# Optimization experiments

Measured on AMD Instinct MI355X. Metric: run time of the kernel, lower is better.

Reference implementation:

```python
import jax, jax.numpy as jnp
import numpy as np

N = 20000
E = 320000
IN_DIM, HID, MID, OUT, HEADS = 1536, 512, 128, 5, 8
NEG_SLOPE = 0.2
BN_EPS = 1e-5


def gat_conv(x, edge_index, W, a_src, a_dst, bias, heads, out_ch):
    """PyG-style GATConv (eval mode, self-loops already in edge_index).
    x: [N, F_in]; W: [F_in, heads*out_ch]; a_src/a_dst: [heads, out_ch]; bias: [heads*out_ch].
    Returns [N, heads*out_ch] (head concat)."""
    n = x.shape[0]
    h = (x @ W).reshape(n, heads, out_ch)              # [N,H,C]
    src, dst = edge_index[0], edge_index[1]
    al_s = jnp.sum(h * a_src, axis=-1)                 # [N,H]
    al_d = jnp.sum(h * a_dst, axis=-1)                 # [N,H]
    e = al_s[src] + al_d[dst]                          # [E,H]
    e = jnp.where(e >= 0, e, NEG_SLOPE * e)            # leaky_relu
    # segment softmax over incoming edges per dst node
    e_max = jax.ops.segment_max(e, dst, num_segments=n)
    e_max = jnp.where(jnp.isfinite(e_max), e_max, 0.0)
    ex = jnp.exp(e - e_max[dst])                       # [E,H]
    denom = jax.ops.segment_sum(ex, dst, num_segments=n)
    alpha = ex / (denom[dst] + 1e-16)                  # [E,H]
    msg = h[src] * alpha[:, :, None]                   # [E,H,C]
    out = jax.ops.segment_sum(msg, dst, num_segments=n)
    return out.reshape(n, heads * out_ch) + bias


def bn_eval(x, gamma, beta, mean, var):
    return (x - mean) * jax.lax.rsqrt(var + BN_EPS) * gamma + beta


def setup_inputs() -> dict:
    key = jax.random.key(0)
    ks = jax.random.split(key, 24)
    x = jax.random.normal(ks[0], (N, IN_DIM), dtype=jnp.float32)
    edge_index = jax.random.randint(ks[1], (2, E), 0, N, dtype=jnp.int32)

    def glorot(k, shape):
        fan = shape[0] + shape[-1]
        return jax.random.normal(k, shape, dtype=jnp.float32) * np.sqrt(2.0 / fan)

    inp = {"x": x, "edge_index": edge_index}
    # conv1: 1536 -> 8 heads x 64
    inp["W1"] = glorot(ks[2], (IN_DIM, HID))
    inp["as1"] = glorot(ks[3], (HEADS, HID // HEADS))
    inp["ad1"] = glorot(ks[4], (HEADS, HID // HEADS))
    inp["b1"] = jnp.zeros((HID,), jnp.float32)
    # conv2: 512 -> 8 heads x 16
    inp["W2"] = glorot(ks[5], (HID, MID))
    inp["as2"] = glorot(ks[6], (HEADS, MID // HEADS))
    inp["ad2"] = glorot(ks[7], (HEADS, MID // HEADS))
    inp["b2"] = jnp.zeros((MID,), jnp.float32)
    # conv3: 128 -> 1 head x 5
    inp["W3"] = glorot(ks[8], (MID, OUT))
    inp["as3"] = glorot(ks[9], (1, OUT))
    inp["ad3"] = glorot(ks[10], (1, OUT))
    inp["b3"] = jnp.zeros((OUT,), jnp.float32)
    # batchnorm params (eval mode, running stats)
    inp["g1"] = jax.random.normal(ks[11], (HID,), jnp.float32) * 0.1 + 1.0
    inp["be1"] = jax.random.normal(ks[12], (HID,), jnp.float32) * 0.1
    inp["m1"] = jax.random.normal(ks[13], (HID,), jnp.float32) * 0.1
    inp["v1"] = jax.random.uniform(ks[14], (HID,), jnp.float32, 0.5, 1.5)
    inp["g2"] = jax.random.normal(ks[15], (MID,), jnp.float32) * 0.1 + 1.0
    inp["be2"] = jax.random.normal(ks[16], (MID,), jnp.float32) * 0.1
    inp["m2"] = jax.random.normal(ks[17], (MID,), jnp.float32) * 0.1
    inp["v2"] = jax.random.uniform(ks[18], (MID,), jnp.float32, 0.5, 1.5)
    return inp


def reference(x, edge_index, W1, as1, ad1, b1, W2, as2, ad2, b2, W3, as3, ad3, b3,
              g1, be1, m1, v1, g2, be2, m2, v2):
    # add self-loops (PyG GATConv default)
    loops = jnp.arange(N, dtype=edge_index.dtype)
    ei = jnp.concatenate([edge_index, jnp.stack([loops, loops])], axis=1)

    h = jax.nn.relu(gat_conv(x, ei, W1, as1, ad1, b1, HEADS, HID // HEADS))
    h = bn_eval(h, g1, be1, m1, v1)
    h = jax.nn.relu(gat_conv(h, ei, W2, as2, ad2, b2, HEADS, MID // HEADS))
    h = bn_eval(h, g2, be2, m2, v2)
    h = gat_conv(h, ei, W3, as3, ad3, b3, 1, OUT)
    return jax.nn.log_softmax(h, axis=1)
```

## Files before the change

kernel.cpp:

```cpp
#include <hip/hip_runtime.h>
#include <math.h>

#define IN_DIM 1536
#define HID 512
#define MID 128
#define OUTC 5
#define HEADS 8
#define NEG_SLOPE 0.2f
#define BN_EPS 1e-5f

typedef __attribute__((ext_vector_type(8))) short s16x8;
typedef __attribute__((ext_vector_type(4))) float fx4;

__device__ __forceinline__ unsigned short bf16_rne(float f) {
    unsigned int u = __float_as_uint(f);
    u += 0x7fffu + ((u >> 16) & 1u);
    return (unsigned short)(u >> 16);
}
__device__ __forceinline__ float bf16_to_f32(unsigned short u) {
    return __uint_as_float((unsigned int)u << 16);
}

__device__ __forceinline__ void async_copy16(void* lds, const void* g) {
    __builtin_amdgcn_global_load_lds(
        (const __attribute__((address_space(1))) unsigned int*)g,
        (__attribute__((address_space(3))) unsigned int*)lds, 16, 0, 0);
}

__global__ void hist_kernel(const int* __restrict__ ei, int* __restrict__ deg,
                            int ET, int E) {
    int e = blockIdx.x * blockDim.x + threadIdx.x;
    if (e >= ET) return;
    int dst = (e < E) ? ei[E + e] : (e - E);
    atomicAdd(&deg[dst], 1);
}

__global__ __launch_bounds__(1024) void scan_kernel(const int* __restrict__ deg,
                                                    int* __restrict__ row_ptr,
                                                    int* __restrict__ cursor, int n) {
    __shared__ int partial[1024];
    int tid = threadIdx.x;
    int per = (n + 1023) / 1024;
    int base = tid * per;
    int s = 0;
    for (int i = 0; i < per; ++i) {
        int idx = base + i;
        if (idx < n) s += deg[idx];
    }
    partial[tid] = s;
    __syncthreads();
    for (int off = 1; off < 1024; off <<= 1) {
        int v = (tid >= off) ? partial[tid - off] : 0;
        __syncthreads();
        partial[tid] += v;
        __syncthreads();
    }
    int prefix = (tid == 0) ? 0 : partial[tid - 1];
    for (int i = 0; i < per; ++i) {
        int idx = base + i;
        if (idx < n) {
            row_ptr[idx] = prefix;
            cursor[idx] = prefix;
            prefix += deg[idx];
        }
    }
    if (tid == 1023) row_ptr[n] = partial[1023];
}

__global__ void scatter_kernel(const int* __restrict__ ei, int* __restrict__ cursor,
                               int* __restrict__ csr_src, int ET, int E) {
    int e = blockIdx.x * blockDim.x + threadIdx.x;
    if (e >= ET) return;
    int src, dst;
    if (e < E) { src = ei[e]; dst = ei[E + e]; }
    else       { src = dst = e - E; }
    int slot = atomicAdd(&cursor[dst], 1);
    csr_src[slot] = src;
}

__global__ void cvt_bf16_kernel(const float* __restrict__ in,
                                unsigned short* __restrict__ out, int n4) {
    int i = blockIdx.x * blockDim.x + threadIdx.x;
    if (i >= n4) return;
    float4 v = ((const float4*)in)[i];
    ushort4 o;
    o.x = bf16_rne(v.x); o.y = bf16_rne(v.y);
    o.z = bf16_rne(v.z); o.w = bf16_rne(v.w);
    ((ushort4*)out)[i] = o;
}

template <bool WLO>
__global__ __launch_bounds__(256) void transpose_split(
    const float* __restrict__ W, unsigned short* __restrict__ Th,
    unsigned short* __restrict__ Tl, int K, int Nn) {
    __shared__ float tile[32][33];
    int kb = blockIdx.y * 32, nb = blockIdx.x * 32;
    int tx = threadIdx.x & 31, ty = threadIdx.x >> 5;
#pragma unroll
    for (int r = 0; r < 4; ++r)
        tile[ty + r * 8][tx] = W[(size_t)(kb + ty + r * 8) * Nn + nb + tx];
    __syncthreads();
#pragma unroll
    for (int r = 0; r < 4; ++r) {
        int n = ty + r * 8;
        float v = tile[tx][n];
        unsigned short hi = bf16_rne(v);
        size_t o = (size_t)(nb + n) * K + kb + tx;
        Th[o] = hi;
        if (WLO) {
            float hif = __uint_as_float((unsigned int)hi << 16);
            Tl[o] = bf16_rne(v - hif);
        }
    }
}

__global__ __launch_bounds__(256) void gemm1_kernel(
    const unsigned short* __restrict__ A, const unsigned short* __restrict__ Bh,
    unsigned short* __restrict__ Cb, int M, int N, int K, int MBLK) {
    int b = blockIdx.x;
    int xm = (b & 7) + 8 * (b >> 5);
    int ym = (b >> 3) & 3;
    if (xm >= MBLK) return;

    __shared__ unsigned short Asb[2][128 * 32];
    __shared__ unsigned short Bsb[2][128 * 32];

    const int tid = threadIdx.x;
    const int lane = tid & 63;
    const int wv = tid >> 6;
    const int row0 = xm * 128;
    const int nb0 = ym * 128;
    const int col = lane & 15;
    const int quad = lane >> 4;
    const int m0 = (wv >> 1) * 64;
    const int n0 = (wv & 1) * 64;

    const int s_row = lane >> 2;
    const int s_chunk = (lane & 3) ^ ((lane >> 3) & 3);
    int agr0 = row0 + (wv * 2 + 0) * 16 + s_row; if (agr0 >= M) agr0 = M - 1;
    int agr1 = row0 + (wv * 2 + 1) * 16 + s_row; if (agr1 >= M) agr1 = M - 1;
    const size_t ag0 = (size_t)agr0 * K + s_chunk * 8;
    const size_t ag1 = (size_t)agr1 * K + s_chunk * 8;
    const size_t bg0 = (size_t)(nb0 + (wv * 2 + 0) * 16 + s_row) * K + s_chunk * 8;
    const size_t bg1 = (size_t)(nb0 + (wv * 2 + 1) * 16 + s_row) * K + s_chunk * 8;

    const int rsw = (col >> 1) & 3;

    fx4 acc[4][4];
#pragma unroll
    for (int i = 0; i < 4; ++i)
#pragma unroll
        for (int j = 0; j < 4; ++j) acc[i][j] = (fx4){0.f, 0.f, 0.f, 0.f};

    async_copy16(&Asb[0][(wv * 2 + 0) * 512], A + ag0);
    async_copy16(&Asb[0][(wv * 2 + 1) * 512], A + ag1);
    async_copy16(&Bsb[0][(wv * 2 + 0) * 512], Bh + bg0);
    async_copy16(&Bsb[0][(wv * 2 + 1) * 512], Bh + bg1);
    __syncthreads();

    int cur = 0;
    for (int k0 = 0; k0 < K; k0 += 32) {
        const int nxt = cur ^ 1;
        if (k0 + 32 < K) {
            const int kn = k0 + 32;
            async_copy16(&Asb[nxt][(wv * 2 + 0) * 512], A + ag0 + kn);
            async_copy16(&Asb[nxt][(wv * 2 + 1) * 512], A + ag1 + kn);
            async_copy16(&Bsb[nxt][(wv * 2 + 0) * 512], Bh + bg0 + kn);
            async_copy16(&Bsb[nxt][(wv * 2 + 1) * 512], Bh + bg1 + kn);
        }
        s16x8 afr[4], bfr[4];
#pragma unroll
        for (int i = 0; i < 4; ++i)
            afr[i] = *(const s16x8*)&Asb[cur][(m0 + i * 16 + col) * 32 + (quad ^ rsw) * 8];
#pragma unroll
        for (int j = 0; j < 4; ++j)
            bfr[j] = *(const s16x8*)&Bsb[cur][(n0 + j * 16 + col) * 32 + (quad ^ rsw) * 8];
#pragma unroll
        for (int i = 0; i < 4; ++i)
#pragma unroll
            for (int j = 0; j < 4; ++j)
                acc[i][j] = __builtin_amdgcn_mfma_f32_16x16x32_bf16(afr[i], bfr[j], acc[i][j], 0, 0, 0);
        __syncthreads();
        cur = nxt;
    }

#pragma unroll
    for (int i = 0; i < 4; ++i) {
        int gr0 = row0 + m0 + i * 16 + quad * 4;
#pragma unroll
        for (int j = 0; j < 4; ++j) {
            int gc = nb0 + n0 + j * 16 + col;
#pragma unroll
            for (int r = 0; r < 4; ++r) {
                int gr = gr0 + r;
                if (gr < M) Cb[(size_t)gr * N + gc] = bf16_rne(acc[i][j][r]);
            }
        }
    }
}

__global__ __launch_bounds__(256) void gemm2_kernel(
    const unsigned short* __restrict__ A, const unsigned short* __restrict__ Bh,
    const unsigned short* __restrict__ Bl, unsigned short* __restrict__ Cb,
    int M, int N, int K) {
    __shared__ unsigned short Asb[2][32 * 32];
    __shared__ unsigned short Bhb[2][128 * 32];
    __shared__ unsigned short Blb[2][128 * 32];

    const int tid = threadIdx.x;
    const int lane = tid & 63;
    const int wv = tid >> 6;
    const int row0 = blockIdx.x * 32;
    const int col = lane & 15;
    const int quad = lane >> 4;
    const int m0 = (wv >> 1) * 16;
    const int n0 = (wv & 1) * 64;
    const int b_row = lane >> 2;
    const int b_chunk = (lane & 3) ^ ((lane >> 3) & 3);
    const int rsw = (col >> 1) & 3;

    const int t0 = wv * 2, t1 = t0 + 1;
    const size_t bgo0 = (size_t)(t0 * 16 + b_row) * K + b_chunk * 8;
    const size_t bgo1 = (size_t)(t1 * 16 + b_row) * K + b_chunk * 8;
    int agr = row0 + wv * 16 + b_row; if (agr >= M) agr = M - 1;
    const size_t ago = (size_t)agr * K + b_chunk * 8;

    fx4 acc[4];
#pragma unroll
    for (int j = 0; j < 4; ++j) acc[j] = (fx4){0.f, 0.f, 0.f, 0.f};

    auto stage = [&](int buf, int k) {
        async_copy16(&Bhb[buf][t0 * 512], Bh + bgo0 + k);
        async_copy16(&Bhb[buf][t1 * 512], Bh + bgo1 + k);
        async_copy16(&Blb[buf][t0 * 512], Bl + bgo0 + k);
        async_copy16(&Blb[buf][t1 * 512], Bl + bgo1 + k);
        if (wv < 2) async_copy16(&Asb[buf][wv * 512], A + ago + k);
    };

    stage(0, 0);
    __syncthreads();

    int cur = 0;
    for (int k0 = 0; k0 < K; k0 += 32) {
        const int nxt = cur ^ 1;
        if (k0 + 32 < K) stage(nxt, k0 + 32);
        s16x8 a, bh4[4], bl4[4];
        a = *(const s16x8*)&Asb[cur][(m0 + col) * 32 + (quad ^ rsw) * 8];
#pragma unroll
        for (int j = 0; j < 4; ++j) {
            int rb = (n0 + j * 16 + col) * 32 + (quad ^ rsw) * 8;
            bh4[j] = *(const s16x8*)&Bhb[cur][rb];
            bl4[j] = *(const s16x8*)&Blb[cur][rb];
        }
#pragma unroll
        for (int j = 0; j < 4; ++j) {
            acc[j] = __builtin_amdgcn_mfma_f32_16x16x32_bf16(a, bl4[j], acc[j], 0, 0, 0);
            acc[j] = __builtin_amdgcn_mfma_f32_16x16x32_bf16(a, bh4[j], acc[j], 0, 0, 0);
        }
        __syncthreads();
        cur = nxt;
    }

    int gr0 = row0 + m0 + quad * 4;
#pragma unroll
    for (int j = 0; j < 4; ++j) {
        int gc = n0 + j * 16 + col;
#pragma unroll
        for (int r = 0; r < 4; ++r) {
            int gr = gr0 + r;
            if (gr < M) Cb[(size_t)gr * N + gc] = bf16_rne(acc[j][r]);
        }
    }
}

template <int H, int C>
__global__ void alsd_kernel(const unsigned short* __restrict__ hlin,
                            const float* __restrict__ a_s,
                            const float* __restrict__ a_d, float* __restrict__ als,
                            float* __restrict__ ald, int n) {
    int t = blockIdx.x * blockDim.x + threadIdx.x;
    if (t >= n * H) return;
    int node = t / H, h = t % H;
    const unsigned short* row = hlin + (size_t)node * H * C + h * C;
    const float* asr = a_s + h * C;
    const float* adr = a_d + h * C;
    float ss = 0.f, sd = 0.f;
#pragma unroll
    for (int c0 = 0; c0 < C; c0 += 4) {
        ushort4 u = *(const ushort4*)&row[c0];
        float v0 = bf16_to_f32(u.x), v1 = bf16_to_f32(u.y);
        float v2 = bf16_to_f32(u.z), v3 = bf16_to_f32(u.w);
        ss += v0 * asr[c0] + v1 * asr[c0 + 1] + v2 * asr[c0 + 2] + v3 * asr[c0 + 3];
        sd += v0 * adr[c0] + v1 * adr[c0 + 1] + v2 * adr[c0 + 2] + v3 * adr[c0 + 3];
    }
    als[t] = ss;
    ald[t] = sd;
}

template <int F, int VEC, bool SPLIT>
__global__ __launch_bounds__(128) void agg_fused_kernel(
    const unsigned short* __restrict__ hlin, const float* __restrict__ als,
    const float* __restrict__ ald, const int* __restrict__ row_ptr,
    const int* __restrict__ csr_src, const float* __restrict__ bias,
    const float* __restrict__ gamma, const float* __restrict__ beta,
    const float* __restrict__ mean, const float* __restrict__ var,
    float* __restrict__ outf, unsigned short* __restrict__ outh) {
    int dst = blockIdx.x;
    int tid = threadIdx.x;
    int f0 = tid * VEC;
    int h = tid >> 4;
    __shared__ float exs[16][8];
    __shared__ int srcs[16];
    int s0 = row_ptr[dst], s1 = row_ptr[dst + 1];
    int cj = tid >> 3, ch = tid & 7;
    float ald_c = ald[dst * HEADS + ch];
    float acc[VEC];
#pragma unroll
    for (int v = 0; v < VEC; ++v) acc[v] = 0.f;
    float den = 0.f;

    for (int base = s0; base < s1; base += 16) {
        int take = min(16, s1 - base);
        if (cj < take) {
            int src = csr_src[base + cj];
            if (ch == 0) srcs[cj] = src;
            float e = als[src * HEADS + ch] + ald_c;
            e = (e >= 0.f) ? e : NEG_SLOPE * e;
            exs[cj][ch] = __expf(e);
        }
        __syncthreads();
        for (int jj = 0; jj < take; ++jj) {
            int src = srcs[jj];
            float a = exs[jj][h];
            den += a;
            const unsigned short* rp = &hlin[(size_t)src * F + f0];
            if (VEC == 4) {
                ushort4 u = *(const ushort4*)rp;
                acc[0] += a * bf16_to_f32(u.x);
                acc[1] += a * bf16_to_f32(u.y);
                acc[2] += a * bf16_to_f32(u.z);
                acc[3] += a * bf16_to_f32(u.w);
            } else {
                acc[0] += a * bf16_to_f32(rp[0]);
            }
        }
        __syncthreads();
    }

    float rd = 1.f / (den + 1e-16f);
    float res[VEC];
#pragma unroll
    for (int v = 0; v < VEC; ++v) {
        int f = f0 + v;
        float val = acc[v] * rd + bias[f];
        val = fmaxf(val, 0.f);
        val = (val - mean[f]) * rsqrtf(var[f] + BN_EPS) * gamma[f] + beta[f];
        res[v] = val;
    }
    if (SPLIT) {
        if (VEC == 4) {
            ushort4 o;
            o.x = bf16_rne(res[0]); o.y = bf16_rne(res[1]);
            o.z = bf16_rne(res[2]); o.w = bf16_rne(res[3]);
            *(ushort4*)&outh[(size_t)dst * F + f0] = o;
        } else {
            outh[(size_t)dst * F + f0] = bf16_rne(res[0]);
        }
    } else {
        if (VEC == 4) {
            *(float4*)&outf[(size_t)dst * F + f0] =
                make_float4(res[0], res[1], res[2], res[3]);
        } else {
            outf[(size_t)dst * F + f0] = res[0];
        }
    }
}

__global__ void layer3_lin_kernel(const float* __restrict__ h2, const float* __restrict__ W3,
                                  const float* __restrict__ as3, const float* __restrict__ ad3,
                                  float* __restrict__ h3lin, float* __restrict__ als,
                                  float* __restrict__ ald, int n) {
    int node = blockIdx.x * blockDim.x + threadIdx.x;
    if (node >= n) return;
    const float* row = h2 + (size_t)node * MID;
    float acc[OUTC] = {0.f, 0.f, 0.f, 0.f, 0.f};
    for (int k = 0; k < MID; ++k) {
        float x = row[k];
#pragma unroll
        for (int c = 0; c < OUTC; ++c) acc[c] += x * W3[k * OUTC + c];
    }
    float ss = 0.f, sd = 0.f;
#pragma unroll
    for (int c = 0; c < OUTC; ++c) {
        h3lin[(size_t)node * OUTC + c] = acc[c];
        ss += acc[c] * as3[c];
        sd += acc[c] * ad3[c];
    }
    als[node] = ss;
    ald[node] = sd;
}

__global__ void agg3_lsm_kernel(const float* __restrict__ h3lin, const float* __restrict__ als,
                                const float* __restrict__ ald, const int* __restrict__ row_ptr,
                                const int* __restrict__ csr_src, const float* __restrict__ b3,
                                float* __restrict__ out, int n) {
    int dst = blockIdx.x * blockDim.x + threadIdx.x;
    if (dst >= n) return;
    int s0 = row_ptr[dst], s1 = row_ptr[dst + 1];
    float ad = ald[dst];
    float den = 0.f;
    float acc[OUTC] = {0.f, 0.f, 0.f, 0.f, 0.f};
    for (int j = s0; j < s1; ++j) {
        int src = csr_src[j];
        float e = als[src] + ad;
        e = (e >= 0.f) ? e : NEG_SLOPE * e;
        float x = __expf(e);
        den += x;
#pragma unroll
        for (int c = 0; c < OUTC; ++c) acc[c] += x * h3lin[(size_t)src * OUTC + c];
    }
    float rd = 1.f / (den + 1e-16f);
    float m = -INFINITY;
#pragma unroll
    for (int c = 0; c < OUTC; ++c) {
        acc[c] = acc[c] * rd + b3[c];
        m = fmaxf(m, acc[c]);
    }
    float s = 0.f;
#pragma unroll
    for (int c = 0; c < OUTC; ++c) s += __expf(acc[c] - m);
    float lse = m + __logf(s);
#pragma unroll
    for (int c = 0; c < OUTC; ++c) out[(size_t)dst * OUTC + c] = acc[c] - lse;
}

extern "C" void kernel_launch(void* const* d_in, const int* in_sizes, int n_in,
                              void* d_out, int out_size, void* d_ws, size_t ws_size,
                              hipStream_t stream) {
    const float* x   = (const float*)d_in[0];
    const int*   ei  = (const int*)d_in[1];
    const float* W1  = (const float*)d_in[2];
    const float* as1 = (const float*)d_in[3];
    const float* ad1 = (const float*)d_in[4];
    const float* b1  = (const float*)d_in[5];
    const float* W2  = (const float*)d_in[6];
    const float* as2 = (const float*)d_in[7];
    const float* ad2 = (const float*)d_in[8];
    const float* b2  = (const float*)d_in[9];
    const float* W3  = (const float*)d_in[10];
    const float* as3 = (const float*)d_in[11];
    const float* ad3 = (const float*)d_in[12];
    const float* b3  = (const float*)d_in[13];
    const float* g1  = (const float*)d_in[14];
    const float* be1 = (const float*)d_in[15];
    const float* m1  = (const float*)d_in[16];
    const float* v1  = (const float*)d_in[17];
    const float* g2  = (const float*)d_in[18];
    const float* be2 = (const float*)d_in[19];
    const float* m2  = (const float*)d_in[20];
    const float* v2  = (const float*)d_in[21];

    const int N = in_sizes[0] / IN_DIM;
    const int E = in_sizes[1] / 2;
    const int ET = E + N;
    const int MBLK1 = (N + 127) / 128;
    const int MBLK2 = (N + 31) / 32;

    char* ws = (char*)d_ws;
    size_t off = 0;
    auto take = [&](size_t bytes) -> char* {
        char* p = ws + off;
        off += (bytes + 255) & ~(size_t)255;
        return p;
    };
    int* deg      = (int*)take((size_t)N * 4);
    int* row_ptr  = (int*)take((size_t)(N + 1) * 4);
    int* cursor   = (int*)take((size_t)N * 4);
    int* csr_src  = (int*)take((size_t)ET * 4);
    unsigned short* W1h = (unsigned short*)take((size_t)HID * IN_DIM * 2);
    unsigned short* W2h = (unsigned short*)take((size_t)MID * HID * 2);
    unsigned short* W2l = (unsigned short*)take((size_t)MID * HID * 2);
    unsigned short* xh  = (unsigned short*)take((size_t)N * IN_DIM * 2);
    unsigned short* h1lin = (unsigned short*)take((size_t)N * HID * 2);
    unsigned short* h1h   = (unsigned short*)take((size_t)N * HID * 2);
    unsigned short* h2lin = (unsigned short*)take((size_t)N * MID * 2);
    float* h2post = (float*)take((size_t)N * MID * 4);
    float* h3lin  = (float*)take((size_t)N * OUTC * 4);
    float* als    = (float*)take((size_t)N * HEADS * 4);
    float* ald    = (float*)take((size_t)N * HEADS * 4);

    hipMemsetAsync(deg, 0, (size_t)N * 4, stream);
    hist_kernel<<<(ET + 255) / 256, 256, 0, stream>>>(ei, deg, ET, E);
    scan_kernel<<<1, 1024, 0, stream>>>(deg, row_ptr, cursor, N);
    scatter_kernel<<<(ET + 255) / 256, 256, 0, stream>>>(ei, cursor, csr_src, ET, E);
    transpose_split<false><<<dim3(HID / 32, IN_DIM / 32), 256, 0, stream>>>(
        W1, W1h, nullptr, IN_DIM, HID);
    transpose_split<true><<<dim3(MID / 32, HID / 32), 256, 0, stream>>>(
        W2, W2h, W2l, HID, MID);
    {
        int n4 = N * IN_DIM / 4;
        cvt_bf16_kernel<<<(n4 + 255) / 256, 256, 0, stream>>>(x, xh, n4);
    }

    gemm1_kernel<<<640, 256, 0, stream>>>(xh, W1h, h1lin, N, HID, IN_DIM, MBLK1);
    alsd_kernel<HEADS, 64><<<(N * HEADS + 255) / 256, 256, 0, stream>>>(h1lin, as1, ad1, als, ald, N);
    agg_fused_kernel<HID, 4, true><<<N, 128, 0, stream>>>(
        h1lin, als, ald, row_ptr, csr_src, b1, g1, be1, m1, v1, nullptr, h1h);

    gemm2_kernel<<<MBLK2, 256, 0, stream>>>(h1h, W2h, W2l, h2lin, N, MID, HID);
    alsd_kernel<HEADS, 16><<<(N * HEADS + 255) / 256, 256, 0, stream>>>(h2lin, as2, ad2, als, ald, N);
    agg_fused_kernel<MID, 1, false><<<N, 128, 0, stream>>>(
        h2lin, als, ald, row_ptr, csr_src, b2, g2, be2, m2, v2, h2post, nullptr);

    layer3_lin_kernel<<<(N + 255) / 256, 256, 0, stream>>>(
        h2post, W3, as3, ad3, h3lin, als, ald, N);
    agg3_lsm_kernel<<<(N + 255) / 256, 256, 0, stream>>>(
        h3lin, als, ald, row_ptr, csr_src, b3, (float*)d_out, N);
}
```

Measured before the change: 467.4 us.

## Fuse attention logits into GEMM epilogues and layer-3 linear into layer-2 aggregation

```diff
diff --git a/kernel.cpp b/kernel.cpp
--- a/kernel.cpp
+++ b/kernel.cpp
@@ -116,7 +116,9 @@
 
 __global__ __launch_bounds__(256) void gemm1_kernel(
     const unsigned short* __restrict__ A, const unsigned short* __restrict__ Bh,
-    unsigned short* __restrict__ Cb, int M, int N, int K, int MBLK) {
+    unsigned short* __restrict__ Cb, const float* __restrict__ a_s,
+    const float* __restrict__ a_d, float* __restrict__ als,
+    float* __restrict__ ald, int M, int N, int K, int MBLK) {
     int b = blockIdx.x;
     int xm = (b & 7) + 8 * (b >> 5);
     int ym = (b >> 3) & 3;
@@ -197,12 +199,43 @@
             }
         }
     }
+
+    const int head = (nb0 + n0) >> 6;
+    float asv[4], adv[4];
+#pragma unroll
+    for (int j = 0; j < 4; ++j) {
+        asv[j] = a_s[head * 64 + j * 16 + col];
+        adv[j] = a_d[head * 64 + j * 16 + col];
+    }
+#pragma unroll
+    for (int i = 0; i < 4; ++i) {
+#pragma unroll
+        for (int r = 0; r < 4; ++r) {
+            float ss = acc[i][0][r] * asv[0] + acc[i][1][r] * asv[1] +
+                       acc[i][2][r] * asv[2] + acc[i][3][r] * asv[3];
+            float sd = acc[i][0][r] * adv[0] + acc[i][1][r] * adv[1] +
+                       acc[i][2][r] * adv[2] + acc[i][3][r] * adv[3];
+#pragma unroll
+            for (int off = 8; off; off >>= 1) {
+                ss += __shfl_xor(ss, off);
+                sd += __shfl_xor(sd, off);
+            }
+            if (col == 0) {
+                int gr = row0 + m0 + i * 16 + quad * 4 + r;
+                if (gr < M) {
+                    als[gr * HEADS + head] = ss;
+                    ald[gr * HEADS + head] = sd;
+                }
+            }
+        }
+    }
 }
 
 __global__ __launch_bounds__(256) void gemm2_kernel(
     const unsigned short* __restrict__ A, const unsigned short* __restrict__ Bh,
     const unsigned short* __restrict__ Bl, unsigned short* __restrict__ Cb,
-    int M, int N, int K) {
+    const float* __restrict__ a_s, const float* __restrict__ a_d,
+    float* __restrict__ als, float* __restrict__ ald, int M, int N, int K) {
     __shared__ unsigned short Asb[2][32 * 32];
     __shared__ unsigned short Bhb[2][128 * 32];
     __shared__ unsigned short Blb[2][128 * 32];
@@ -271,40 +304,44 @@
             if (gr < M) Cb[(size_t)gr * N + gc] = bf16_rne(acc[j][r]);
         }
     }
-}
-
-template <int H, int C>
-__global__ void alsd_kernel(const unsigned short* __restrict__ hlin,
-                            const float* __restrict__ a_s,
-                            const float* __restrict__ a_d, float* __restrict__ als,
-                            float* __restrict__ ald, int n) {
-    int t = blockIdx.x * blockDim.x + threadIdx.x;
-    if (t >= n * H) return;
-    int node = t / H, h = t % H;
-    const unsigned short* row = hlin + (size_t)node * H * C + h * C;
-    const float* asr = a_s + h * C;
-    const float* adr = a_d + h * C;
-    float ss = 0.f, sd = 0.f;
-#pragma unroll
-    for (int c0 = 0; c0 < C; c0 += 4) {
-        ushort4 u = *(const ushort4*)&row[c0];
-        float v0 = bf16_to_f32(u.x), v1 = bf16_to_f32(u.y);
-        float v2 = bf16_to_f32(u.z), v3 = bf16_to_f32(u.w);
-        ss += v0 * asr[c0] + v1 * asr[c0 + 1] + v2 * asr[c0 + 2] + v3 * asr[c0 + 3];
-        sd += v0 * adr[c0] + v1 * adr[c0 + 1] + v2 * adr[c0 + 2] + v3 * adr[c0 + 3];
-    }
-    als[t] = ss;
-    ald[t] = sd;
-}
-
-template <int F, int VEC, bool SPLIT>
+
+    float asv[4], adv[4];
+#pragma unroll
+    for (int j = 0; j < 4; ++j) {
+        asv[j] = a_s[n0 + j * 16 + col];
+        adv[j] = a_d[n0 + j * 16 + col];
+    }
+#pragma unroll
+    for (int j = 0; j < 4; ++j) {
+        int head = (n0 >> 4) + j;
+#pragma unroll
+        for (int r = 0; r < 4; ++r) {
+            float ss = acc[j][r] * asv[j];
+            float sd = acc[j][r] * adv[j];
+#pragma unroll
+            for (int off = 8; off; off >>= 1) {
+                ss += __shfl_xor(ss, off);
+                sd += __shfl_xor(sd, off);
+            }
+            if (col == 0) {
+                int gr = gr0 + r;
+                if (gr < M) {
+                    als[gr * HEADS + head] = ss;
+                    ald[gr * HEADS + head] = sd;
+                }
+            }
+        }
+    }
+}
+
+template <int F, int VEC>
 __global__ __launch_bounds__(128) void agg_fused_kernel(
     const unsigned short* __restrict__ hlin, const float* __restrict__ als,
     const float* __restrict__ ald, const int* __restrict__ row_ptr,
     const int* __restrict__ csr_src, const float* __restrict__ bias,
     const float* __restrict__ gamma, const float* __restrict__ beta,
     const float* __restrict__ mean, const float* __restrict__ var,
-    float* __restrict__ outf, unsigned short* __restrict__ outh) {
+    unsigned short* __restrict__ outh) {
     int dst = blockIdx.x;
     int tid = threadIdx.x;
     int f0 = tid * VEC;
@@ -334,104 +371,144 @@
             float a = exs[jj][h];
             den += a;
             const unsigned short* rp = &hlin[(size_t)src * F + f0];
-            if (VEC == 4) {
-                ushort4 u = *(const ushort4*)rp;
-                acc[0] += a * bf16_to_f32(u.x);
-                acc[1] += a * bf16_to_f32(u.y);
-                acc[2] += a * bf16_to_f32(u.z);
-                acc[3] += a * bf16_to_f32(u.w);
-            } else {
-                acc[0] += a * bf16_to_f32(rp[0]);
-            }
+            ushort4 u = *(const ushort4*)rp;
+            acc[0] += a * bf16_to_f32(u.x);
+            acc[1] += a * bf16_to_f32(u.y);
+            acc[2] += a * bf16_to_f32(u.z);
+            acc[3] += a * bf16_to_f32(u.w);
         }
         __syncthreads();
     }
 
     float rd = 1.f / (den + 1e-16f);
-    float res[VEC];
+    ushort4 o;
+    unsigned short* op = (unsigned short*)&o;
 #pragma unroll
     for (int v = 0; v < VEC; ++v) {
         int f = f0 + v;
         float val = acc[v] * rd + bias[f];
         val = fmaxf(val, 0.f);
         val = (val - mean[f]) * rsqrtf(var[f] + BN_EPS) * gamma[f] + beta[f];
-        res[v] = val;
-    }
-    if (SPLIT) {
-        if (VEC == 4) {
-            ushort4 o;
-            o.x = bf16_rne(res[0]); o.y = bf16_rne(res[1]);
-            o.z = bf16_rne(res[2]); o.w = bf16_rne(res[3]);
-            *(ushort4*)&outh[(size_t)dst * F + f0] = o;
-        } else {
-            outh[(size_t)dst * F + f0] = bf16_rne(res[0]);
-        }
-    } else {
-        if (VEC == 4) {
-            *(float4*)&outf[(size_t)dst * F + f0] =
-                make_float4(res[0], res[1], res[2], res[3]);
-        } else {
-            outf[(size_t)dst * F + f0] = res[0];
-        }
-    }
-}
-
-__global__ void layer3_lin_kernel(const float* __restrict__ h2, const float* __restrict__ W3,
-                                  const float* __restrict__ as3, const float* __restrict__ ad3,
-                                  float* __restrict__ h3lin, float* __restrict__ als,
-                                  float* __restrict__ ald, int n) {
-    int node = blockIdx.x * blockDim.x + threadIdx.x;
-    if (node >= n) return;
-    const float* row = h2 + (size_t)node * MID;
-    float acc[OUTC] = {0.f, 0.f, 0.f, 0.f, 0.f};
-    for (int k = 0; k < MID; ++k) {
-        float x = row[k];
-#pragma unroll
-        for (int c = 0; c < OUTC; ++c) acc[c] += x * W3[k * OUTC + c];
-    }
-    float ss = 0.f, sd = 0.f;
-#pragma unroll
-    for (int c = 0; c < OUTC; ++c) {
-        h3lin[(size_t)node * OUTC + c] = acc[c];
-        ss += acc[c] * as3[c];
-        sd += acc[c] * ad3[c];
-    }
-    als[node] = ss;
-    ald[node] = sd;
-}
-
-__global__ void agg3_lsm_kernel(const float* __restrict__ h3lin, const float* __restrict__ als,
-                                const float* __restrict__ ald, const int* __restrict__ row_ptr,
-                                const int* __restrict__ csr_src, const float* __restrict__ b3,
-                                float* __restrict__ out, int n) {
-    int dst = blockIdx.x * blockDim.x + threadIdx.x;
+        op[v] = bf16_rne(val);
+    }
+    *(ushort4*)&outh[(size_t)dst * F + f0] = o;
+}
+
+__global__ __launch_bounds__(128) void agg2_l3_kernel(
+    const unsigned short* __restrict__ hlin, const float* __restrict__ als,
+    const float* __restrict__ ald, const int* __restrict__ row_ptr,
+    const int* __restrict__ csr_src, const float* __restrict__ bias,
+    const float* __restrict__ gamma, const float* __restrict__ beta,
+    const float* __restrict__ mean, const float* __restrict__ var,
+    const float* __restrict__ W3, const float* __restrict__ as3,
+    const float* __restrict__ ad3, float* __restrict__ h3lin,
+    float* __restrict__ als3, float* __restrict__ ald3) {
+    int dst = blockIdx.x;
+    int tid = threadIdx.x;
+    int h = tid >> 4;
+    __shared__ float exs[16][8];
+    __shared__ int srcs[16];
+    __shared__ float red[2][OUTC];
+    int s0 = row_ptr[dst], s1 = row_ptr[dst + 1];
+    int cj = tid >> 3, ch = tid & 7;
+    float ald_c = ald[dst * HEADS + ch];
+    float acc = 0.f, den = 0.f;
+
+    for (int base = s0; base < s1; base += 16) {
+        int take = min(16, s1 - base);
+        if (cj < take) {
+            int src = csr_src[base + cj];
+            if (ch == 0) srcs[cj] = src;
+            float e = als[src * HEADS + ch] + ald_c;
+            e = (e >= 0.f) ? e : NEG_SLOPE * e;
+            exs[cj][ch] = __expf(e);
+        }
+        __syncthreads();
+        for (int jj = 0; jj < take; ++jj) {
+            int src = srcs[jj];
+            float a = exs[jj][h];
+            den += a;
+            acc += a * bf16_to_f32(hlin[(size_t)src * MID + tid]);
+        }
+        __syncthreads();
+    }
+
+    float val = acc / (den + 1e-16f) + bias[tid];
+    val = fmaxf(val, 0.f);
+    val = (val - mean[tid]) * rsqrtf(var[tid] + BN_EPS) * gamma[tid] + beta[tid];
+
+    float p[OUTC];
+#pragma unroll
+    for (int c = 0; c < OUTC; ++c) p[c] = val * W3[tid * OUTC + c];
+#pragma unroll
+    for (int off = 32; off; off >>= 1) {
+#pragma unroll
+        for (int c = 0; c < OUTC; ++c) p[c] += __shfl_xor(p[c], off);
+    }
+    int wv = tid >> 6;
+    if ((tid & 63) == 0) {
+#pragma unroll
+        for (int c = 0; c < OUTC; ++c) red[wv][c] = p[c];
+    }
+    __syncthreads();
+    if (tid == 0) {
+        float ss = 0.f, sd = 0.f;
+#pragma unroll
+        for (int c = 0; c < OUTC; ++c) {
+            float v = red[0][c] + red[1][c];
+            h3lin[(size_t)dst * OUTC + c] = v;
+            ss += v * as3[c];
+            sd += v * ad3[c];
+        }
+        als3[dst] = ss;
+        ald3[dst] = sd;
+    }
+}
+
+__global__ __launch_bounds__(256) void agg3_lsm_kernel(
+    const float* __restrict__ h3lin, const float* __restrict__ als,
+    const float* __restrict__ ald, const int* __restrict__ row_ptr,
+    const int* __restrict__ csr_src, const float* __restrict__ b3,
+    float* __restrict__ out, int n) {
+    int g = blockIdx.x * blockDim.x + threadIdx.x;
+    int dst = g >> 4;
+    int l = g & 15;
     if (dst >= n) return;
     int s0 = row_ptr[dst], s1 = row_ptr[dst + 1];
     float ad = ald[dst];
     float den = 0.f;
     float acc[OUTC] = {0.f, 0.f, 0.f, 0.f, 0.f};
-    for (int j = s0; j < s1; ++j) {
+    for (int j = s0 + l; j < s1; j += 16) {
         int src = csr_src[j];
         float e = als[src] + ad;
         e = (e >= 0.f) ? e : NEG_SLOPE * e;
         float x = __expf(e);
         den += x;
-#pragma unroll
-        for (int c = 0; c < OUTC; ++c) acc[c] += x * h3lin[(size_t)src * OUTC + c];
-    }
-    float rd = 1.f / (den + 1e-16f);
-    float m = -INFINITY;
-#pragma unroll
-    for (int c = 0; c < OUTC; ++c) {
-        acc[c] = acc[c] * rd + b3[c];
-        m = fmaxf(m, acc[c]);
-    }
-    float s = 0.f;
-#pragma unroll
-    for (int c = 0; c < OUTC; ++c) s += __expf(acc[c] - m);
-    float lse = m + __logf(s);
-#pragma unroll
-    for (int c = 0; c < OUTC; ++c) out[(size_t)dst * OUTC + c] = acc[c] - lse;
+        const float* hp = h3lin + (size_t)src * OUTC;
+#pragma unroll
+        for (int c = 0; c < OUTC; ++c) acc[c] += x * hp[c];
+    }
+#pragma unroll
+    for (int off = 8; off; off >>= 1) {
+        den += __shfl_xor(den, off);
+#pragma unroll
+        for (int c = 0; c < OUTC; ++c) acc[c] += __shfl_xor(acc[c], off);
+    }
+    if (l == 0) {
+        float rd = 1.f / (den + 1e-16f);
+        float m = -INFINITY;
+#pragma unroll
+        for (int c = 0; c < OUTC; ++c) {
+            acc[c] = acc[c] * rd + b3[c];
+            m = fmaxf(m, acc[c]);
+        }
+        float s = 0.f;
+#pragma unroll
+        for (int c = 0; c < OUTC; ++c) s += __expf(acc[c] - m);
+        float lse = m + __logf(s);
+#pragma unroll
+        for (int c = 0; c < OUTC; ++c) out[(size_t)dst * OUTC + c] = acc[c] - lse;
+    }
 }
 
 extern "C" void kernel_launch(void* const* d_in, const int* in_sizes, int n_in,
@@ -484,10 +561,11 @@
     unsigned short* h1lin = (unsigned short*)take((size_t)N * HID * 2);
     unsigned short* h1h   = (unsigned short*)take((size_t)N * HID * 2);
     unsigned short* h2lin = (unsigned short*)take((size_t)N * MID * 2);
-    float* h2post = (float*)take((size_t)N * MID * 4);
     float* h3lin  = (float*)take((size_t)N * OUTC * 4);
     float* als    = (float*)take((size_t)N * HEADS * 4);
     float* ald    = (float*)take((size_t)N * HEADS * 4);
+    float* als3   = (float*)take((size_t)N * 4);
+    float* ald3   = (float*)take((size_t)N * 4);
 
     hipMemsetAsync(deg, 0, (size_t)N * 4, stream);
     hist_kernel<<<(ET + 255) / 256, 256, 0, stream>>>(ei, deg, ET, E);
@@ -502,18 +580,17 @@
         cvt_bf16_kernel<<<(n4 + 255) / 256, 256, 0, stream>>>(x, xh, n4);
     }
 
-    gemm1_kernel<<<640, 256, 0, stream>>>(xh, W1h, h1lin, N, HID, IN_DIM, MBLK1);
-    alsd_kernel<HEADS, 64><<<(N * HEADS + 255) / 256, 256, 0, stream>>>(h1lin, as1, ad1, als, ald, N);
-    agg_fused_kernel<HID, 4, true><<<N, 128, 0, stream>>>(
-        h1lin, als, ald, row_ptr, csr_src, b1, g1, be1, m1, v1, nullptr, h1h);
-
-    gemm2_kernel<<<MBLK2, 256, 0, stream>>>(h1h, W2h, W2l, h2lin, N, MID, HID);
-    alsd_kernel<HEADS, 16><<<(N * HEADS + 255) / 256, 256, 0, stream>>>(h2lin, as2, ad2, als, ald, N);
-    agg_fused_kernel<MID, 1, false><<<N, 128, 0, stream>>>(
-        h2lin, als, ald, row_ptr, csr_src, b2, g2, be2, m2, v2, h2post, nullptr);
-
-    layer3_lin_kernel<<<(N + 255) / 256, 256, 0, stream>>>(
-        h2post, W3, as3, ad3, h3lin, als, ald, N);
-    agg3_lsm_kernel<<<(N + 255) / 256, 256, 0, stream>>>(
-        h3lin, als, ald, row_ptr, csr_src, b3, (float*)d_out, N);
-}
+    gemm1_kernel<<<640, 256, 0, stream>>>(xh, W1h, h1lin, as1, ad1, als, ald,
+                                          N, HID, IN_DIM, MBLK1);
+    agg_fused_kernel<HID, 4><<<N, 128, 0, stream>>>(
+        h1lin, als, ald, row_ptr, csr_src, b1, g1, be1, m1, v1, h1h);
+
+    gemm2_kernel<<<MBLK2, 256, 0, stream>>>(h1h, W2h, W2l, h2lin, as2, ad2,
+                                            als, ald, N, MID, HID);
+    agg2_l3_kernel<<<N, 128, 0, stream>>>(
+        h2lin, als, ald, row_ptr, csr_src, b2, g2, be2, m2, v2,
+        W3, as3, ad3, h3lin, als3, ald3);
+
+    agg3_lsm_kernel<<<(N * 16 + 255) / 256, 256, 0, stream>>>(
+        h3lin, als3, ald3, row_ptr, csr_src, b3, (float*)d_out, N);
+}
```

Result: faster. 446.0 us (-4.6%).
